# Performance work log

Hardware: AMD Instinct MI355X
Metric: run time of the kernel (lower is better)

## Reference

```python
import jax, jax.numpy as jnp
import numpy as np

L, H, DH, D, F, BLK, VOCAB = 2, 16, 128, 2048, 8192, 64, 32000
B, S, R = 16, 77, 16
LORA_SCALE = 32.0 / 16.0  # alpha / r

# standard bitsandbytes NF4 codebook
NF4 = jnp.array([-1.0, -0.6961928009986877, -0.5250730514526367,
                 -0.39491748809814453, -0.28444138169288635, -0.18477343022823334,
                 -0.09105003625154495, 0.0, 0.07958029955625534, 0.16093020141124725,
                 0.24611230194568634, 0.33791524171829224, 0.44070982933044434,
                 0.5626170039176941, 0.723855197429657, 1.0], dtype=jnp.float32)


def setup_inputs() -> dict:
    key = jax.random.key(0)
    ks = jax.random.split(key, 24)
    n = lambda k, sh, s=0.02: jax.random.normal(k, sh, jnp.float32) * s
    u = lambda k, sh: jax.random.uniform(k, sh, dtype=jnp.float32) * 0.02
    ri = lambda k, sh, hi: jax.random.randint(k, sh, 0, hi, jnp.int32)
    return {
        "input_ids": ri(ks[0], (B, S), VOCAB),
        "attention_mask": jnp.ones((B, S), jnp.int32),
        "embed": n(ks[1], (VOCAB, D)),
        "ln_attn": jnp.ones((L, D), jnp.float32),
        "ln_mlp": jnp.ones((L, D), jnp.float32),
        "ln_final": jnp.ones((D,), jnp.float32),
        "qkv_codes": ri(ks[2], (L, 3, D, D), 16),
        "qkv_absmax": u(ks[3], (L, 3, D, D // BLK)),
        "qkv_A": n(ks[4], (L, 3, R, D)),
        "qkv_B": n(ks[5], (L, 3, D, R), 0.01),
        "o_codes": ri(ks[6], (L, D, D), 16),
        "o_absmax": u(ks[7], (L, D, D // BLK)),
        "o_A": n(ks[8], (L, R, D)),
        "o_B": n(ks[9], (L, D, R), 0.01),
        "gu_codes": ri(ks[10], (L, 2, F, D), 16),
        "gu_absmax": u(ks[11], (L, 2, F, D // BLK)),
        "gu_A": n(ks[12], (L, 2, R, D)),
        "gu_B": n(ks[13], (L, 2, F, R), 0.01),
        "down_codes": ri(ks[14], (L, D, F), 16),
        "down_absmax": u(ks[15], (L, D, F // BLK)),
        "down_A": n(ks[16], (L, R, F)),
        "down_B": n(ks[17], (L, D, R), 0.01),
    }


def _rmsnorm(x, w, eps=1e-6):
    return x * jax.lax.rsqrt(jnp.mean(x * x, axis=-1, keepdims=True) + eps) * w


def _dequant(codes, absmax):
    # codes: (out, cin) ints in [0,16); absmax: (out, cin//BLK) blockwise scales
    out, cin = codes.shape
    w = NF4[codes].reshape(out, cin // BLK, BLK) * absmax[..., None]
    return w.reshape(out, cin)


def _qlora(x, codes, absmax, A, Bm):
    # NF4 dequant base matmul + rank-R LoRA delta (eval mode, no dropout)
    W = _dequant(codes, absmax)
    return x @ W.T + LORA_SCALE * ((x @ A.T) @ Bm.T)


def _rope_cache(seq):
    inv = 1.0 / (10000.0 ** (jnp.arange(0, DH, 2, dtype=jnp.float32) / DH))
    f = jnp.arange(seq, dtype=jnp.float32)[:, None] * inv  # (S, DH/2)
    emb = jnp.concatenate([f, f], axis=-1)                 # (S, DH)
    return jnp.cos(emb), jnp.sin(emb)


def _rope(x, cos, sin):
    # x: (B, H, S, DH), llama-style rotate_half
    x1, x2 = jnp.split(x, 2, axis=-1)
    return x * cos + jnp.concatenate([-x2, x1], axis=-1) * sin


def _forward(input_ids, attention_mask, embed, ln_attn, ln_mlp, ln_final,
             qkv_codes, qkv_absmax, qkv_A, qkv_B,
             o_codes, o_absmax, o_A, o_B,
             gu_codes, gu_absmax, gu_A, gu_B,
             down_codes, down_absmax, down_A, down_B):
    b, s = input_ids.shape
    h = embed[input_ids]                                    # (B, S, D)
    cos, sin = _rope_cache(s)
    pad = attention_mask.astype(bool)[:, None, None, :]     # (B,1,1,S)
    mask = pad & jnp.tril(jnp.ones((s, s), bool))
    inv_sqrt_dh = np.float32(1.0 / np.sqrt(DH))
    for l in range(L):
        x = _rmsnorm(h, ln_attn[l])
        q, k, v = [_qlora(x, qkv_codes[l, i], qkv_absmax[l, i], qkv_A[l, i], qkv_B[l, i])
                   .reshape(b, s, H, DH).transpose(0, 2, 1, 3) for i in range(3)]
        q, k = _rope(q, cos, sin), _rope(k, cos, sin)
        scores = jnp.einsum('bhqd,bhkd->bhqk', q, k) * inv_sqrt_dh
        attn = jax.nn.softmax(jnp.where(mask, scores, -1e9), axis=-1)
        o = jnp.einsum('bhqk,bhkd->bhqd', attn, v).transpose(0, 2, 1, 3).reshape(b, s, D)
        h = h + _qlora(o, o_codes[l], o_absmax[l], o_A[l], o_B[l])
        x = _rmsnorm(h, ln_mlp[l])
        g = _qlora(x, gu_codes[l, 0], gu_absmax[l, 0], gu_A[l, 0], gu_B[l, 0])
        up = _qlora(x, gu_codes[l, 1], gu_absmax[l, 1], gu_A[l, 1], gu_B[l, 1])
        h = h + _qlora(jax.nn.silu(g) * up,
                       down_codes[l], down_absmax[l], down_A[l], down_B[l])
    h = _rmsnorm(h, ln_final)
    lengths = attention_mask.sum(axis=1) - 1                # last non-pad token index
    return h[jnp.arange(b), lengths]                        # (B, D)


def reference(input_ids, attention_mask, embed, ln_attn, ln_mlp, ln_final,
              qkv_codes, qkv_absmax, qkv_A, qkv_B,
              o_codes, o_absmax, o_A, o_B,
              gu_codes, gu_absmax, gu_A, gu_B,
              down_codes, down_absmax, down_A, down_B):
    return _forward(input_ids, attention_mask, embed, ln_attn, ln_mlp, ln_final,
                    qkv_codes, qkv_absmax, qkv_A, qkv_B,
                    o_codes, o_absmax, o_A, o_B,
                    gu_codes, gu_absmax, gu_A, gu_B,
                    down_codes, down_absmax, down_A, down_B)
```

## Files before the change

kernel.cpp:

```cpp
#include <hip/hip_runtime.h>
#include <cstdint>
#include <cstddef>

#define M_TOK   1232
#define M_PAD   1280
#define D_MODEL 2048
#define F_FFN   8192
#define SEQ     77
#define BATCH   16
#define NHEAD   16
#define LRANK   16
#define NLAYER  2
#define ATILE   16
#define MWB     512

typedef short bf16x8 __attribute__((ext_vector_type(8)));
typedef float f32x4  __attribute__((ext_vector_type(4)));

__device__ __constant__ float NF4C[16] = {
  -1.0f, -0.6961928009986877f, -0.5250730514526367f, -0.39491748809814453f,
  -0.28444138169288635f, -0.18477343022823334f, -0.09105003625154495f, 0.0f,
  0.07958029955625534f, 0.16093020141124725f, 0.24611230194568634f,
  0.33791524171829224f, 0.44070982933044434f, 0.5626170039176941f,
  0.723855197429657f, 1.0f };

__device__ inline unsigned short f2b(float f) {
  unsigned u = __builtin_bit_cast(unsigned, f);
  u += 0x7FFFu + ((u >> 16) & 1u);
  return (unsigned short)(u >> 16);
}
__device__ inline float b2f(unsigned short s) {
  return __builtin_bit_cast(float, ((unsigned)s) << 16);
}

__global__ __launch_bounds__(256) void mat_w(
    const int* __restrict__ C, const float* __restrict__ AM,
    unsigned short* __restrict__ W, int K, long total8, int ilv)
{
  __shared__ float tb[16];
  if (threadIdx.x < 16) tb[threadIdx.x] = NF4C[threadIdx.x];
  __syncthreads();
  const int KB = K >> 6;
  for (long i = (long)blockIdx.x * 256 + threadIdx.x; i < total8;
       i += (long)gridDim.x * 256) {
    long e = i << 3;
    int rd = (int)(e / K), k = (int)(e - (long)rd * K);
    int srcn = ilv ? ((rd & 1) * F_FFN + (rd >> 1)) : rd;
    float am = AM[(size_t)srcn * KB + (k >> 6)];
    const int4* cp = (const int4*)(C + (size_t)srcn * K + k);
    int4 a = cp[0], b = cp[1];
    uint4 o;
    o.x = (unsigned)f2b(tb[a.x] * am) | ((unsigned)f2b(tb[a.y] * am) << 16);
    o.y = (unsigned)f2b(tb[a.z] * am) | ((unsigned)f2b(tb[a.w] * am) << 16);
    o.z = (unsigned)f2b(tb[b.x] * am) | ((unsigned)f2b(tb[b.y] * am) << 16);
    o.w = (unsigned)f2b(tb[b.z] * am) | ((unsigned)f2b(tb[b.w] * am) << 16);
    *(uint4*)(W + e) = o;
  }
}

__global__ __launch_bounds__(256, 2) void gemm_bf(
    const unsigned short* __restrict__ X, const unsigned short* __restrict__ W,
    float* __restrict__ O, int mb, int N, int K, int acc_mode, int splitk,
    const float* __restrict__ T, const float* __restrict__ Bm, int sh, int nr,
    int gum, unsigned short* __restrict__ GB,
    const int* __restrict__ C2, const float* __restrict__ AM2,
    unsigned short* __restrict__ W2, int K2, long total8_2, int ilv2, int Ggemm)
{
  __shared__ __align__(16) unsigned short xs[128 * 64];
  __shared__ __align__(16) unsigned short ws[128 * 64];

  int tid = threadIdx.x;

  if ((int)blockIdx.x >= Ggemm) {
    if (total8_2 > 0) {
      float* tb = (float*)xs;
      if (tid < 16) tb[tid] = NF4C[tid];
      __syncthreads();
      int nblk2 = gridDim.x - Ggemm;
      const int KB2 = K2 >> 6;
      for (long i = (long)((int)blockIdx.x - Ggemm) * 256 + tid; i < total8_2;
           i += (long)nblk2 * 256) {
        long e = i << 3;
        int rd = (int)(e / K2), k = (int)(e - (long)rd * K2);
        int srcn = ilv2 ? ((rd & 1) * F_FFN + (rd >> 1)) : rd;
        float am = AM2[(size_t)srcn * KB2 + (k >> 6)];
        const int4* cp = (const int4*)(C2 + (size_t)srcn * K2 + k);
        int4 a = cp[0], b = cp[1];
        uint4 o;
        o.x = (unsigned)f2b(tb[a.x] * am) | ((unsigned)f2b(tb[a.y] * am) << 16);
        o.y = (unsigned)f2b(tb[a.z] * am) | ((unsigned)f2b(tb[a.w] * am) << 16);
        o.z = (unsigned)f2b(tb[b.x] * am) | ((unsigned)f2b(tb[b.y] * am) << 16);
        o.w = (unsigned)f2b(tb[b.z] * am) | ((unsigned)f2b(tb[b.w] * am) << 16);
        *(uint4*)(W2 + e) = o;
      }
    }
    return;
  }

  int nwg = Ggemm;
  int q8 = nwg >> 3, r8 = nwg & 7;
  int xcd = blockIdx.x & 7, pos = blockIdx.x >> 3;
  int wgid = (xcd < r8) ? (xcd * (q8 + 1) + pos)
                        : (r8 * (q8 + 1) + (xcd - r8) * q8 + pos);
  int nb = N >> 7;
  int per = mb * nb;
  int slice = wgid / per; int rem = wgid - slice * per;
  int nblk = rem / mb, mblk = rem - nblk * mb;
  int row0 = mblk << 7, col0 = nblk << 7;
  int KBtot = K >> 6, kcnt = KBtot / splitk, kbeg = slice * kcnt;

  int wave = tid >> 6, lane = tid & 63;
  int fr = lane & 15, fg = lane >> 4, s7 = fr & 7;
  int wm = (wave >> 1) * 64, wn = (wave & 1) * 64;
  int xg = lane >> 3;
  int xcol = (((lane & 7) ^ (xg & 7)) << 3);

  const unsigned short* Xbase = X + (size_t)row0 * K + (size_t)kbeg * 64;
  const unsigned short* Wbase = W + (size_t)col0 * K + (size_t)kbeg * 64;

  f32x4 accm[4][4];
  #pragma unroll
  for (int i = 0; i < 4; ++i)
    #pragma unroll
    for (int j = 0; j < 4; ++j) accm[i][j] = (f32x4){0.f, 0.f, 0.f, 0.f};

  auto stage = [&](int t) {
    const unsigned short* xb = Xbase + (size_t)t * 64;
    const unsigned short* wb = Wbase + (size_t)t * 64;
    #pragma unroll
    for (int p2 = 0; p2 < 4; ++p2) {
      int c = wave * 4 + p2;
      const unsigned short* gp = xb + (size_t)(c * 8 + xg) * K + xcol;
      __builtin_amdgcn_global_load_lds(
          (const __attribute__((address_space(1))) unsigned int*)gp,
          (__attribute__((address_space(3))) unsigned int*)(xs + c * 512),
          16, 0, 0);
    }
    #pragma unroll
    for (int p2 = 0; p2 < 4; ++p2) {
      int c = wave * 4 + p2;
      const unsigned short* gp = wb + (size_t)(c * 8 + xg) * K + xcol;
      __builtin_amdgcn_global_load_lds(
          (const __attribute__((address_space(1))) unsigned int*)gp,
          (__attribute__((address_space(3))) unsigned int*)(ws + c * 512),
          16, 0, 0);
    }
  };
  auto compute = [&]() {
    bf16x8 b0[4], b1[4];
    #pragma unroll
    for (int ni = 0; ni < 4; ++ni) {
      const unsigned short* wr = ws + (wn + ni * 16 + fr) * 64;
      b0[ni] = *(const bf16x8*)(wr + ((fg ^ s7) << 3));
      b1[ni] = *(const bf16x8*)(wr + (((4 | fg) ^ s7) << 3));
    }
    #pragma unroll
    for (int mi = 0; mi < 4; ++mi) {
      const unsigned short* xr = xs + (wm + mi * 16 + fr) * 64;
      bf16x8 a0 = *(const bf16x8*)(xr + ((fg ^ s7) << 3));
      bf16x8 a1 = *(const bf16x8*)(xr + (((4 | fg) ^ s7) << 3));
      #pragma unroll
      for (int ni = 0; ni < 4; ++ni) {
        accm[mi][ni] = __builtin_amdgcn_mfma_f32_16x16x32_bf16(
            a0, b0[ni], accm[mi][ni], 0, 0, 0);
        accm[mi][ni] = __builtin_amdgcn_mfma_f32_16x16x32_bf16(
            a1, b1[ni], accm[mi][ni], 0, 0, 0);
      }
    }
  };

  stage(0);
  for (int t = 0; t < kcnt; ++t) {
    __syncthreads();
    compute();
    if (t + 1 < kcnt) {
      __syncthreads();
      stage(t + 1);
    }
  }

  if (gum) {
    float* Tt = (float*)&xs[0];
    float* Bt = (float*)&ws[0];
    __syncthreads();
    for (int idx = tid; idx < 128 * 32; idx += 256) {
      int rr = idx >> 5, c = idx & 31;
      int gm = row0 + rr;
      Tt[idx] = (gm < M_TOK) ? T[(size_t)gm * 32 + c] : 0.f;
    }
    for (int idx = tid; idx < 128 * 16; idx += 256) {
      int rr = idx >> 4, c = idx & 15;
      int type = rr & 1, nrow = (col0 + rr) >> 1;
      Bt[idx] = Bm[((size_t)type * F_FFN + nrow) * LRANK + c];
    }
    __syncthreads();
    #pragma unroll
    for (int mi = 0; mi < 4; ++mi)
      #pragma unroll
      for (int ni = 0; ni < 4; ++ni) {
        int gm0 = row0 + wm + mi * 16 + fg * 4;
        int gnl = wn + ni * 16 + fr;
        #pragma unroll
        for (int r = 0; r < 4; ++r) {
          int gm = gm0 + r;
          float vv = accm[mi][ni][r];
          const float* tr = Tt + (wm + mi * 16 + fg * 4 + r) * 32 + ((gnl & 1) << 4);
          const float* br = Bt + gnl * 16;
          float s = 0.f;
          #pragma unroll
          for (int c = 0; c < 16; ++c) s += tr[c] * br[c];
          vv += 2.0f * s;
          float prt = __shfl_xor(vv, 1);
          if (gm < M_TOK && !(fr & 1)) {
            float sig = 1.0f / (1.0f + expf(-vv));
            GB[(size_t)gm * F_FFN + ((col0 + gnl) >> 1)] = f2b(vv * sig * prt);
          }
        }
      }
    return;
  }

  int doT = (T != nullptr) && (slice == 0);
  float* Tt = (float*)&xs[0];
  float* Bt = (float*)&ws[0];
  if (doT) {
    __syncthreads();
    int toff = (col0 >> sh) << 4;
    for (int idx = tid; idx < 128 * 16; idx += 256) {
      int rr = idx >> 4, c = idx & 15;
      int gm = row0 + rr;
      Tt[idx] = (gm < M_TOK) ? T[(size_t)gm * nr + toff + c] : 0.f;
      Bt[idx] = Bm[(size_t)(col0 + rr) * LRANK + c];
    }
    __syncthreads();
  }

  #pragma unroll
  for (int mi = 0; mi < 4; ++mi)
    #pragma unroll
    for (int ni = 0; ni < 4; ++ni) {
      int gm0 = row0 + wm + mi * 16 + fg * 4;
      int gnl = wn + ni * 16 + fr;
      int gn = col0 + gnl;
      #pragma unroll
      for (int r = 0; r < 4; ++r) {
        int gm = gm0 + r;
        if (gm < M_TOK) {
          size_t idx = (size_t)gm * N + gn;
          float vv = accm[mi][ni][r];
          if (doT) {
            const float* tr = Tt + (wm + mi * 16 + fg * 4 + r) * 16;
            const float* br = Bt + gnl * 16;
            float s = 0.f;
            #pragma unroll
            for (int c = 0; c < 16; ++c) s += tr[c] * br[c];
            vv += 2.0f * s;
          }
          if (splitk > 1)       atomicAdd(&O[idx], vv);
          else if (acc_mode)    O[idx] += vv;
          else                  O[idx] = vv;
        }
      }
    }
}

__global__ __launch_bounds__(256) void lora1(
    const unsigned short* __restrict__ X, const float* __restrict__ A,
    float* __restrict__ T, int K)
{
  int m0 = blockIdx.x * 4, bi = blockIdx.y, nmat = gridDim.y;
  int g = threadIdx.x >> 4, l16 = threadIdx.x & 15;
  const float* ar = A + (size_t)bi * LRANK * K + (size_t)g * K;
  const unsigned short* x0 = X + (size_t)m0 * K;
  float s0 = 0.f, s1 = 0.f, s2 = 0.f, s3 = 0.f;
  for (int kk = l16 * 4; kk < K; kk += 64) {
    float4 av = *(const float4*)(ar + kk);
    ushort4 v0 = *(const ushort4*)(x0 + kk);
    ushort4 v1 = *(const ushort4*)(x0 + K + kk);
    ushort4 v2 = *(const ushort4*)(x0 + 2 * K + kk);
    ushort4 v3 = *(const ushort4*)(x0 + 3 * K + kk);
    s0 += b2f(v0.x)*av.x + b2f(v0.y)*av.y + b2f(v0.z)*av.z + b2f(v0.w)*av.w;
    s1 += b2f(v1.x)*av.x + b2f(v1.y)*av.y + b2f(v1.z)*av.z + b2f(v1.w)*av.w;
    s2 += b2f(v2.x)*av.x + b2f(v2.y)*av.y + b2f(v2.z)*av.z + b2f(v2.w)*av.w;
    s3 += b2f(v3.x)*av.x + b2f(v3.y)*av.y + b2f(v3.z)*av.z + b2f(v3.w)*av.w;
  }
  #pragma unroll
  for (int off = 8; off; off >>= 1) {
    s0 += __shfl_down(s0, off, 16);
    s1 += __shfl_down(s1, off, 16);
    s2 += __shfl_down(s2, off, 16);
    s3 += __shfl_down(s3, off, 16);
  }
  if (l16 == 0) {
    size_t base = ((size_t)m0 * nmat + bi) * LRANK + g;
    size_t rs = (size_t)nmat * LRANK;
    T[base] = s0; T[base + rs] = s1; T[base + 2*rs] = s2; T[base + 3*rs] = s3;
  }
}

__global__ __launch_bounds__(256) void rmsnorm_k(
    const float* __restrict__ H, const float* __restrict__ W,
    unsigned short* __restrict__ X, int D)
{
  int m = blockIdx.x;
  const float* hr = H + (size_t)m * D;
  float s = 0.f;
  for (int i = threadIdx.x; i < D; i += 256) { float v = hr[i]; s += v * v; }
  __shared__ float red[4];
  #pragma unroll
  for (int off = 32; off; off >>= 1) s += __shfl_down(s, off, 64);
  if ((threadIdx.x & 63) == 0) red[threadIdx.x >> 6] = s;
  __syncthreads();
  float tot = red[0] + red[1] + red[2] + red[3];
  float inv = rsqrtf(tot / (float)D + 1e-6f);
  for (int i = threadIdx.x; i < D; i += 256)
    X[(size_t)m * D + i] = f2b(hr[i] * inv * W[i]);
}

__global__ void rope_table(float* __restrict__ cosT, float* __restrict__ sinT)
{
  int idx = blockIdx.x * 64 + threadIdx.x;
  if (idx >= SEQ * 64) return;
  int s = idx >> 6, j = idx & 63;
  float inv = powf(10000.0f, -(float)(2 * j) / 128.0f);
  float f = (float)s * inv;
  cosT[idx] = cosf(f);
  sinT[idx] = sinf(f);
}

__global__ __launch_bounds__(256) void attn_k(
    const float* __restrict__ QKV, const int* __restrict__ amask,
    const float* __restrict__ cosT, const float* __restrict__ sinT,
    unsigned short* __restrict__ O)
{
  int bh = blockIdx.x, it = blockIdx.y;
  int b = bh >> 4, h = bh & (NHEAD - 1);
  const int STR = 3 * D_MODEL;
  __shared__ float ks[SEQ * 132];
  __shared__ float qs[ATILE * 132];
  __shared__ float sc[ATILE * 80];
  __shared__ int am[SEQ];
  const float scale = 0.08838834764831845f;

  const float* Kb = QKV + (size_t)(b * SEQ) * STR + D_MODEL + h * 128;
  for (int idx = threadIdx.x; idx < SEQ * 16; idx += 256) {
    int j = idx >> 4, dq = (idx & 15) << 2;
    float4 a = *(const float4*)(Kb + (size_t)j * STR + dq);
    float4 bb = *(const float4*)(Kb + (size_t)j * STR + dq + 64);
    float4 c4 = *(const float4*)(cosT + j * 64 + dq);
    float4 s4 = *(const float4*)(sinT + j * 64 + dq);
    float* kr = ks + j * 132 + dq;
    kr[0] = a.x*c4.x - bb.x*s4.x; kr[1] = a.y*c4.y - bb.y*s4.y;
    kr[2] = a.z*c4.z - bb.z*s4.z; kr[3] = a.w*c4.w - bb.w*s4.w;
    kr[64] = bb.x*c4.x + a.x*s4.x; kr[65] = bb.y*c4.y + a.y*s4.y;
    kr[66] = bb.z*c4.z + a.z*s4.z; kr[67] = bb.w*c4.w + a.w*s4.w;
  }
  const float* Qb = QKV + (size_t)(b * SEQ) * STR + h * 128;
  for (int idx = threadIdx.x; idx < ATILE * 16; idx += 256) {
    int il = idx >> 4, dq = (idx & 15) << 2;
    int i = it * ATILE + il;
    if (i < SEQ) {
      float4 a = *(const float4*)(Qb + (size_t)i * STR + dq);
      float4 bb = *(const float4*)(Qb + (size_t)i * STR + dq + 64);
      float4 c4 = *(const float4*)(cosT + i * 64 + dq);
      float4 s4 = *(const float4*)(sinT + i * 64 + dq);
      float* qr = qs + il * 132 + dq;
      qr[0] = a.x*c4.x - bb.x*s4.x; qr[1] = a.y*c4.y - bb.y*s4.y;
      qr[2] = a.z*c4.z - bb.z*s4.z; qr[3] = a.w*c4.w - bb.w*s4.w;
      qr[64] = bb.x*c4.x + a.x*s4.x; qr[65] = bb.y*c4.y + a.y*s4.y;
      qr[66] = bb.z*c4.z + a.z*s4.z; qr[67] = bb.w*c4.w + a.w*s4.w;
    }
  }
  for (int j = threadIdx.x; j < SEQ; j += 256) am[j] = amask[b * SEQ + j];
  __syncthreads();

  int wave = threadIdx.x >> 6, lane = threadIdx.x & 63;
  #pragma unroll
  for (int r = 0; r < 4; ++r) {
    int il = wave * 4 + r;
    int i = it * ATILE + il;
    if (i < SEQ) {
      const float4* qr = (const float4*)(qs + il * 132);
      int j1 = lane, j2 = lane + 64;
      float v1 = -1e9f, v2 = -1e9f;
      if (j1 <= i && am[j1]) {
        const float4* kr = (const float4*)(ks + j1 * 132);
        float s = 0.f;
        #pragma unroll 8
        for (int d = 0; d < 32; ++d) {
          float4 a = qr[d], c = kr[d];
          s += a.x*c.x + a.y*c.y + a.z*c.z + a.w*c.w;
        }
        v1 = s * scale;
      }
      if (j2 < SEQ && j2 <= i && am[j2]) {
        const float4* kr = (const float4*)(ks + j2 * 132);
        float s = 0.f;
        #pragma unroll 8
        for (int d = 0; d < 32; ++d) {
          float4 a = qr[d], c = kr[d];
          s += a.x*c.x + a.y*c.y + a.z*c.z + a.w*c.w;
        }
        v2 = s * scale;
      }
      float mx = fmaxf(v1, v2);
      #pragma unroll
      for (int off = 32; off; off >>= 1) mx = fmaxf(mx, __shfl_xor(mx, off));
      float e1 = __expf(v1 - mx);
      float e2 = (j2 < SEQ) ? __expf(v2 - mx) : 0.f;
      float sum = e1 + e2;
      #pragma unroll
      for (int off = 32; off; off >>= 1) sum += __shfl_xor(sum, off);
      float inv = 1.0f / sum;
      sc[il * 80 + j1] = e1 * inv;
      if (j2 < SEQ) sc[il * 80 + j2] = e2 * inv;
    }
  }
  __syncthreads();

  const float* Vbase = QKV + (size_t)(b * SEQ) * STR + 2 * D_MODEL + h * 128;
  for (int idx = threadIdx.x; idx < ATILE * 32; idx += 256) {
    int il = idx >> 5, d4 = (idx & 31) << 2;
    int i = it * ATILE + il;
    if (i >= SEQ) continue;
    float4 acc = {0.f, 0.f, 0.f, 0.f};
    const float* sr = sc + il * 80;
    for (int j = 0; j < SEQ; ++j) {
      float pp = sr[j];
      float4 v = *(const float4*)(Vbase + (size_t)j * STR + d4);
      acc.x += pp * v.x; acc.y += pp * v.y; acc.z += pp * v.z; acc.w += pp * v.w;
    }
    unsigned short* op = O + (size_t)(b * SEQ + i) * D_MODEL + h * 128 + d4;
    op[0] = f2b(acc.x); op[1] = f2b(acc.y); op[2] = f2b(acc.z); op[3] = f2b(acc.w);
  }
}

__global__ void embed_gather(const float* __restrict__ E, const int* __restrict__ ids,
                             float* __restrict__ H)
{
  size_t idx = (size_t)blockIdx.x * 256 + threadIdx.x;
  int m = (int)(idx / D_MODEL);
  int n = (int)(idx % D_MODEL);
  H[idx] = E[(size_t)ids[m] * D_MODEL + n];
}

__global__ __launch_bounds__(256) void final_k(
    const float* __restrict__ H, const int* __restrict__ amask,
    const float* __restrict__ W, float* __restrict__ out)
{
  int b = blockIdx.x;
  __shared__ int len;
  if (threadIdx.x == 0) {
    int s = 0;
    for (int j = 0; j < SEQ; ++j) s += amask[b * SEQ + j];
    len = s - 1;
  }
  __syncthreads();
  const float* hr = H + ((size_t)(b * SEQ + len) * D_MODEL);
  float s = 0.f;
  for (int i = threadIdx.x; i < D_MODEL; i += 256) { float v = hr[i]; s += v * v; }
  __shared__ float red[4];
  #pragma unroll
  for (int off = 32; off; off >>= 1) s += __shfl_down(s, off, 64);
  if ((threadIdx.x & 63) == 0) red[threadIdx.x >> 6] = s;
  __syncthreads();
  float tot = red[0] + red[1] + red[2] + red[3];
  float inv = rsqrtf(tot / (float)D_MODEL + 1e-6f);
  for (int i = threadIdx.x; i < D_MODEL; i += 256)
    out[(size_t)b * D_MODEL + i] = hr[i] * inv * W[i];
}

extern "C" void kernel_launch(void* const* d_in, const int* in_sizes, int n_in,
                              void* d_out, int out_size, void* d_ws, size_t ws_size,
                              hipStream_t stream) {
  const int*   ids     = (const int*)d_in[0];
  const int*   amask   = (const int*)d_in[1];
  const float* embed   = (const float*)d_in[2];
  const float* ln_attn = (const float*)d_in[3];
  const float* ln_mlp  = (const float*)d_in[4];
  const float* ln_fin  = (const float*)d_in[5];
  const int*   qkvC    = (const int*)d_in[6];
  const float* qkvS    = (const float*)d_in[7];
  const float* qkvA    = (const float*)d_in[8];
  const float* qkvB    = (const float*)d_in[9];
  const int*   oC      = (const int*)d_in[10];
  const float* oS      = (const float*)d_in[11];
  const float* oA      = (const float*)d_in[12];
  const float* oB      = (const float*)d_in[13];
  const int*   guC     = (const int*)d_in[14];
  const float* guS     = (const float*)d_in[15];
  const float* guA     = (const float*)d_in[16];
  const float* guB     = (const float*)d_in[17];
  const int*   dnC     = (const int*)d_in[18];
  const float* dnS     = (const float*)d_in[19];
  const float* dnA     = (const float*)d_in[20];
  const float* dnB     = (const float*)d_in[21];
  float* out = (float*)d_out;

  const int M = M_TOK, Mp = M_PAD, D = D_MODEL, F = F_FFN, R = LRANK;
  float* p = (float*)d_ws;
  float* h    = p; p += (size_t)Mp * D;
  float* qkv  = p; p += (size_t)Mp * 3 * D;
  float* t    = p; p += (size_t)Mp * 48;
  float* cosT = p; p += SEQ * 64;
  float* sinT = p; p += SEQ * 64;
  unsigned short* xbf = (unsigned short*)p; p += (size_t)Mp * D / 2;
  unsigned short* gbf = (unsigned short*)p; p += (size_t)Mp * F / 2;
  unsigned short* wQ = (unsigned short*)p; p += (size_t)3 * D * D / 2;
  unsigned short* wO = (unsigned short*)p; p += (size_t)D * D / 2;
  unsigned short* wG = (unsigned short*)p; p += (size_t)2 * F * D / 2;
  unsigned short* wD = (unsigned short*)p; p += (size_t)D * F / 2;

  rope_table<<<(SEQ*64 + 63)/64, 64, 0, stream>>>(cosT, sinT);
  embed_gather<<<(M * D)/256, 256, 0, stream>>>(embed, ids, h);
  mat_w<<<2048, 256, 0, stream>>>(qkvC, qkvS, wQ, D, (long)3*D*D/8, 0);

  const int mb = Mp / 128;
  const int Gqkv = mb * (3*D/128);
  const int Go   = mb * (D/128) * 4;
  const int Ggu  = mb * (2*F/128);
  const int Gdn  = mb * (D/128) * 4;

  for (int l = 0; l < NLAYER; ++l) {
    rmsnorm_k<<<M, 256, 0, stream>>>(h, ln_attn + (size_t)l * D, xbf, D);
    lora1<<<dim3(M/4, 3), 256, 0, stream>>>(xbf, qkvA + (size_t)l*3*R*D, t, D);
    gemm_bf<<<Gqkv + MWB, 256, 0, stream>>>(
        xbf, wQ, qkv, mb, 3*D, D, 0, 1,
        t, qkvB + (size_t)l*3*D*R, 11, 48, 0, nullptr,
        oC + (size_t)l*D*D, oS + (size_t)l*D*(D/64), wO, D, (long)D*D/8, 0, Gqkv);
    attn_k<<<dim3(BATCH*NHEAD, (SEQ + ATILE - 1)/ATILE), 256, 0, stream>>>(
        qkv, amask, cosT, sinT, xbf);
    lora1<<<dim3(M/4, 1), 256, 0, stream>>>(xbf, oA + (size_t)l*R*D, t, D);
    gemm_bf<<<Go + MWB, 256, 0, stream>>>(
        xbf, wO, h, mb, D, D, 1, 4,
        t, oB + (size_t)l*D*R, 11, 16, 0, nullptr,
        guC + (size_t)l*2*F*D, guS + (size_t)l*2*F*(D/64), wG, D, (long)2*F*D/8, 1, Go);

    rmsnorm_k<<<M, 256, 0, stream>>>(h, ln_mlp + (size_t)l * D, xbf, D);
    lora1<<<dim3(M/4, 2), 256, 0, stream>>>(xbf, guA + (size_t)l*2*R*D, t, D);
    gemm_bf<<<Ggu + MWB, 256, 0, stream>>>(
        xbf, wG, nullptr, mb, 2*F, D, 0, 1,
        t, guB + (size_t)l*2*F*R, 0, 32, 1, gbf,
        dnC + (size_t)l*D*F, dnS + (size_t)l*D*(F/64), wD, F, (long)D*F/8, 0, Ggu);
    lora1<<<dim3(M/4, 1), 256, 0, stream>>>(gbf, dnA + (size_t)l*R*F, t, F);
    if (l + 1 < NLAYER) {
      gemm_bf<<<Gdn + MWB, 256, 0, stream>>>(
          gbf, wD, h, mb, D, F, 1, 4,
          t, dnB + (size_t)l*D*R, 11, 16, 0, nullptr,
          qkvC + (size_t)(l+1)*3*D*D, qkvS + (size_t)(l+1)*3*D*(D/64),
          wQ, D, (long)3*D*D/8, 0, Gdn);
    } else {
      gemm_bf<<<Gdn, 256, 0, stream>>>(
          gbf, wD, h, mb, D, F, 1, 4,
          t, dnB + (size_t)l*D*R, 11, 16, 0, nullptr,
          nullptr, nullptr, nullptr, D, 0, 0, Gdn);
    }
  }
  final_k<<<BATCH, 256, 0, stream>>>(h, amask, ln_fin, out);
}
```

Measured before the change: 1.158 ms.

## Rebalance NF4 weight dequant across GEMM launches with two carry segments

GEMM kernels could previously dequantize only one upcoming weight matrix in their spare blocks. They can now dequantize two ranges. The QKV GEMM dequantizes the output-projection weights plus the first 5/8 of the gate/up weights, and the output-projection GEMM finishes the rest of gate/up. This spreads the large gate/up dequant over two overlapping launches so no single GEMM carries a heavy tail. The cost is more carry blocks on the QKV launch, which compete with its GEMM work.

New measurement: 1.142 ms. About the same (-1.4%).

```diff
diff --git a/kernel.cpp b/kernel.cpp
--- a/kernel.cpp
+++ b/kernel.cpp
@@ -12,7 +12,6 @@
 #define LRANK   16
 #define NLAYER  2
 #define ATILE   16
-#define MWB     512
 
 typedef short bf16x8 __attribute__((ext_vector_type(8)));
 typedef float f32x4  __attribute__((ext_vector_type(4)));
@@ -33,29 +32,35 @@
   return __builtin_bit_cast(float, ((unsigned)s) << 16);
 }
 
-__global__ __launch_bounds__(256) void mat_w(
-    const int* __restrict__ C, const float* __restrict__ AM,
-    unsigned short* __restrict__ W, int K, long total8, int ilv)
-{
-  __shared__ float tb[16];
-  if (threadIdx.x < 16) tb[threadIdx.x] = NF4C[threadIdx.x];
-  __syncthreads();
-  const int KB = K >> 6;
-  for (long i = (long)blockIdx.x * 256 + threadIdx.x; i < total8;
-       i += (long)gridDim.x * 256) {
-    long e = i << 3;
-    int rd = (int)(e / K), k = (int)(e - (long)rd * K);
-    int srcn = ilv ? ((rd & 1) * F_FFN + (rd >> 1)) : rd;
-    float am = AM[(size_t)srcn * KB + (k >> 6)];
-    const int4* cp = (const int4*)(C + (size_t)srcn * K + k);
+__device__ inline void carry_body(const float* tb, long cid, long ncb, int tid,
+                                  const int* C2, const float* AM2,
+                                  unsigned short* W2, int K2, long beg8,
+                                  long cnt8, int ilv2) {
+  const int KB2 = K2 >> 6;
+  for (long i = cid * 256 + tid; i < cnt8; i += ncb * 256) {
+    long e = (beg8 + i) << 3;
+    int rd = (int)(e / K2), k = (int)(e - (long)rd * K2);
+    int srcn = ilv2 ? ((rd & 1) * F_FFN + (rd >> 1)) : rd;
+    float am = AM2[(size_t)srcn * KB2 + (k >> 6)];
+    const int4* cp = (const int4*)(C2 + (size_t)srcn * K2 + k);
     int4 a = cp[0], b = cp[1];
     uint4 o;
     o.x = (unsigned)f2b(tb[a.x] * am) | ((unsigned)f2b(tb[a.y] * am) << 16);
     o.y = (unsigned)f2b(tb[a.z] * am) | ((unsigned)f2b(tb[a.w] * am) << 16);
     o.z = (unsigned)f2b(tb[b.x] * am) | ((unsigned)f2b(tb[b.y] * am) << 16);
     o.w = (unsigned)f2b(tb[b.z] * am) | ((unsigned)f2b(tb[b.w] * am) << 16);
-    *(uint4*)(W + e) = o;
-  }
+    *(uint4*)(W2 + e) = o;
+  }
+}
+
+__global__ __launch_bounds__(256) void mat_w(
+    const int* __restrict__ C, const float* __restrict__ AM,
+    unsigned short* __restrict__ W, int K, long total8, int ilv)
+{
+  __shared__ float tb[16];
+  if (threadIdx.x < 16) tb[threadIdx.x] = NF4C[threadIdx.x];
+  __syncthreads();
+  carry_body(tb, blockIdx.x, gridDim.x, threadIdx.x, C, AM, W, K, 0, total8, ilv);
 }
 
 __global__ __launch_bounds__(256, 2) void gemm_bf(
@@ -63,8 +68,11 @@
     float* __restrict__ O, int mb, int N, int K, int acc_mode, int splitk,
     const float* __restrict__ T, const float* __restrict__ Bm, int sh, int nr,
     int gum, unsigned short* __restrict__ GB,
+    const int* __restrict__ C1, const float* __restrict__ AM1,
+    unsigned short* __restrict__ W1, int K1, long beg1, long cnt1, int ilv1, int nc1,
     const int* __restrict__ C2, const float* __restrict__ AM2,
-    unsigned short* __restrict__ W2, int K2, long total8_2, int ilv2, int Ggemm)
+    unsigned short* __restrict__ W2, int K2, long beg2, long cnt2, int ilv2,
+    int Ggemm)
 {
   __shared__ __align__(16) unsigned short xs[128 * 64];
   __shared__ __align__(16) unsigned short ws[128 * 64];
@@ -72,27 +80,17 @@
   int tid = threadIdx.x;
 
   if ((int)blockIdx.x >= Ggemm) {
-    if (total8_2 > 0) {
-      float* tb = (float*)xs;
-      if (tid < 16) tb[tid] = NF4C[tid];
-      __syncthreads();
-      int nblk2 = gridDim.x - Ggemm;
-      const int KB2 = K2 >> 6;
-      for (long i = (long)((int)blockIdx.x - Ggemm) * 256 + tid; i < total8_2;
-           i += (long)nblk2 * 256) {
-        long e = i << 3;
-        int rd = (int)(e / K2), k = (int)(e - (long)rd * K2);
-        int srcn = ilv2 ? ((rd & 1) * F_FFN + (rd >> 1)) : rd;
-        float am = AM2[(size_t)srcn * KB2 + (k >> 6)];
-        const int4* cp = (const int4*)(C2 + (size_t)srcn * K2 + k);
-        int4 a = cp[0], b = cp[1];
-        uint4 o;
-        o.x = (unsigned)f2b(tb[a.x] * am) | ((unsigned)f2b(tb[a.y] * am) << 16);
-        o.y = (unsigned)f2b(tb[a.z] * am) | ((unsigned)f2b(tb[a.w] * am) << 16);
-        o.z = (unsigned)f2b(tb[b.x] * am) | ((unsigned)f2b(tb[b.y] * am) << 16);
-        o.w = (unsigned)f2b(tb[b.z] * am) | ((unsigned)f2b(tb[b.w] * am) << 16);
-        *(uint4*)(W2 + e) = o;
-      }
+    int cb = (int)blockIdx.x - Ggemm;
+    float* tb = (float*)xs;
+    if (tid < 16) tb[tid] = NF4C[tid];
+    __syncthreads();
+    if (cb < nc1) {
+      if (cnt1 > 0)
+        carry_body(tb, cb, nc1, tid, C1, AM1, W1, K1, beg1, cnt1, ilv1);
+    } else {
+      int ncb2 = gridDim.x - Ggemm - nc1;
+      if (cnt2 > 0 && ncb2 > 0)
+        carry_body(tb, cb - nc1, ncb2, tid, C2, AM2, W2, K2, beg2, cnt2, ilv2);
     }
     return;
   }
@@ -520,40 +518,51 @@
   const int Go   = mb * (D/128) * 4;
   const int Ggu  = mb * (2*F/128);
   const int Gdn  = mb * (D/128) * 4;
+  const long oT8   = (long)D * D / 8;
+  const long guT8  = (long)2 * F * D / 8;
+  const long guA8  = guT8 * 5 / 8;
+  const long dnT8  = (long)D * F / 8;
+  const long qkvT8 = (long)3 * D * D / 8;
 
   for (int l = 0; l < NLAYER; ++l) {
     rmsnorm_k<<<M, 256, 0, stream>>>(h, ln_attn + (size_t)l * D, xbf, D);
     lora1<<<dim3(M/4, 3), 256, 0, stream>>>(xbf, qkvA + (size_t)l*3*R*D, t, D);
-    gemm_bf<<<Gqkv + MWB, 256, 0, stream>>>(
+    gemm_bf<<<Gqkv + 768, 256, 0, stream>>>(
         xbf, wQ, qkv, mb, 3*D, D, 0, 1,
         t, qkvB + (size_t)l*3*D*R, 11, 48, 0, nullptr,
-        oC + (size_t)l*D*D, oS + (size_t)l*D*(D/64), wO, D, (long)D*D/8, 0, Gqkv);
+        oC + (size_t)l*D*D, oS + (size_t)l*D*(D/64), wO, D, 0, oT8, 0, 192,
+        guC + (size_t)l*2*F*D, guS + (size_t)l*2*F*(D/64), wG, D, 0, guA8, 1, Gqkv);
     attn_k<<<dim3(BATCH*NHEAD, (SEQ + ATILE - 1)/ATILE), 256, 0, stream>>>(
         qkv, amask, cosT, sinT, xbf);
     lora1<<<dim3(M/4, 1), 256, 0, stream>>>(xbf, oA + (size_t)l*R*D, t, D);
-    gemm_bf<<<Go + MWB, 256, 0, stream>>>(
+    gemm_bf<<<Go + 512, 256, 0, stream>>>(
         xbf, wO, h, mb, D, D, 1, 4,
         t, oB + (size_t)l*D*R, 11, 16, 0, nullptr,
-        guC + (size_t)l*2*F*D, guS + (size_t)l*2*F*(D/64), wG, D, (long)2*F*D/8, 1, Go);
+        guC + (size_t)l*2*F*D, guS + (size_t)l*2*F*(D/64), wG, D,
+        guA8, guT8 - guA8, 1, 512,
+        nullptr, nullptr, nullptr, D, 0, 0, 0, Go);
 
     rmsnorm_k<<<M, 256, 0, stream>>>(h, ln_mlp + (size_t)l * D, xbf, D);
     lora1<<<dim3(M/4, 2), 256, 0, stream>>>(xbf, guA + (size_t)l*2*R*D, t, D);
-    gemm_bf<<<Ggu + MWB, 256, 0, stream>>>(
+    gemm_bf<<<Ggu + 512, 256, 0, stream>>>(
         xbf, wG, nullptr, mb, 2*F, D, 0, 1,
         t, guB + (size_t)l*2*F*R, 0, 32, 1, gbf,
-        dnC + (size_t)l*D*F, dnS + (size_t)l*D*(F/64), wD, F, (long)D*F/8, 0, Ggu);
+        dnC + (size_t)l*D*F, dnS + (size_t)l*D*(F/64), wD, F, 0, dnT8, 0, 512,
+        nullptr, nullptr, nullptr, D, 0, 0, 0, Ggu);
     lora1<<<dim3(M/4, 1), 256, 0, stream>>>(gbf, dnA + (size_t)l*R*F, t, F);
     if (l + 1 < NLAYER) {
-      gemm_bf<<<Gdn + MWB, 256, 0, stream>>>(
+      gemm_bf<<<Gdn + 512, 256, 0, stream>>>(
           gbf, wD, h, mb, D, F, 1, 4,
           t, dnB + (size_t)l*D*R, 11, 16, 0, nullptr,
           qkvC + (size_t)(l+1)*3*D*D, qkvS + (size_t)(l+1)*3*D*(D/64),
-          wQ, D, (long)3*D*D/8, 0, Gdn);
+          wQ, D, 0, qkvT8, 0, 512,
+          nullptr, nullptr, nullptr, D, 0, 0, 0, Gdn);
     } else {
       gemm_bf<<<Gdn, 256, 0, stream>>>(
           gbf, wD, h, mb, D, F, 1, 4,
           t, dnB + (size_t)l*D*R, 11, 16, 0, nullptr,
-          nullptr, nullptr, nullptr, D, 0, 0, Gdn);
+          nullptr, nullptr, nullptr, D, 0, 0, 0, 0,
+          nullptr, nullptr, nullptr, D, 0, 0, 0, Gdn);
     }
   }
   final_k<<<BATCH, 256, 0, stream>>>(h, amask, ln_fin, out);
```
